# Performance work log

Hardware: AMD Instinct MI355X
Metric: run time of the kernel (lower is better)

The kernel has to match this reference:

```python
import jax, jax.numpy as jnp
import numpy as np

N_NODES = 50000
N_GRAPHS = 64


def _gcn_layer(x, w, b, src, dst, dinv):
    # GCNConv: out = D^{-1/2} (A+I) D^{-1/2} (x W) + b; self-loops already in src/dst
    xw = x @ w                                  # [N, out]
    norm = (dinv[src] * dinv[dst])[:, None]     # [E+N, 1]
    msgs = xw[src] * norm                       # gather + scale
    out = jax.ops.segment_sum(msgs, dst, num_segments=N_NODES)
    return out + b


def setup_inputs() -> dict:
    key = jax.random.key(0)
    ks = jax.random.split(key, 12)
    E = 800000
    F_IN, H = 128, 256
    x = jax.random.normal(ks[0], (N_NODES, F_IN), dtype=jnp.float32)
    edge_attr = jax.random.normal(ks[1], (E, 4), dtype=jnp.float32)
    edge_index = jax.random.randint(ks[2], (2, E), 0, N_NODES, dtype=jnp.int64)
    batch = jnp.sort(jax.random.randint(ks[3], (N_NODES,), 0, N_GRAPHS, dtype=jnp.int64))
    def glorot(k, fi, fo):
        s = jnp.sqrt(6.0 / (fi + fo))
        return jax.random.uniform(k, (fi, fo), minval=-s, maxval=s, dtype=jnp.float32)
    return {
        "x": x, "edge_attr": edge_attr, "edge_index": edge_index, "batch": batch,
        "w1": glorot(ks[4], F_IN, H), "b1": jnp.zeros((H,), jnp.float32),
        "w2": glorot(ks[5], H, H), "b2": jnp.zeros((H,), jnp.float32),
        "w3": glorot(ks[6], H, H), "b3": jnp.zeros((H,), jnp.float32),
        "lin1_w": glorot(ks[7], H, H // 2), "lin1_b": jnp.zeros((H // 2,), jnp.float32),
        "lin2_w": glorot(ks[8], H // 2, 3), "lin2_b": jnp.zeros((3,), jnp.float32),
    }


def reference(x, edge_attr, edge_index, batch, w1, b1, w2, b2, w3, b3,
              lin1_w, lin1_b, lin2_w, lin2_b):
    # add self-loops once; shared by all three conv layers
    loop = jnp.arange(N_NODES, dtype=edge_index.dtype)
    src = jnp.concatenate([edge_index[0], loop])
    dst = jnp.concatenate([edge_index[1], loop])
    deg = jax.ops.segment_sum(jnp.ones_like(dst, dtype=x.dtype), dst, num_segments=N_NODES)
    dinv = jnp.where(deg > 0, jax.lax.rsqrt(deg), 0.0)

    h = jax.nn.relu(_gcn_layer(x, w1, b1, src, dst, dinv))
    h = jax.nn.relu(_gcn_layer(h, w2, b2, src, dst, dinv))
    h = _gcn_layer(h, w3, b3, src, dst, dinv)

    # global mean pool over graphs
    sums = jax.ops.segment_sum(h, batch, num_segments=N_GRAPHS)
    cnts = jax.ops.segment_sum(jnp.ones((h.shape[0],), h.dtype), batch, num_segments=N_GRAPHS)
    pooled = sums / jnp.maximum(cnts, 1.0)[:, None]

    # eval mode: dropout is identity
    out = pooled @ lin1_w + lin1_b
    out = out @ lin2_w + lin2_b
    return out
```

## Files before the change

kernel.cpp:

```cpp
#include <hip/hip_runtime.h>
#include <cstdint>

constexpr int NG = 64;
constexpr int H  = 256;

typedef __bf16 bf16x8 __attribute__((ext_vector_type(8)));
typedef float  f32x4  __attribute__((ext_vector_type(4)));

__device__ __forceinline__ uint32_t pk_bf16(float a, float b) {
    uint32_t ua = __builtin_bit_cast(uint32_t, a);
    uint32_t ub = __builtin_bit_cast(uint32_t, b);
    ua += 0x7fffu + ((ua >> 16) & 1u);
    ub += 0x7fffu + ((ub >> 16) & 1u);
    return (ua >> 16) | (ub & 0xffff0000u);
}
__device__ __forceinline__ ushort bf16r(float x) {
    uint32_t u = __builtin_bit_cast(uint32_t, x);
    u += 0x7fffu + ((u >> 16) & 1u);
    return (ushort)(u >> 16);
}
__device__ __forceinline__ float bf2f(ushort h) {
    return __builtin_bit_cast(float, ((uint32_t)h) << 16);
}
__device__ __forceinline__ void bf2acc(uint32_t u, float& a0, float& a1) {
    a0 += __builtin_bit_cast(float, u << 16);
    a1 += __builtin_bit_cast(float, u & 0xffff0000u);
}

__global__ void hist_kernel(const int* __restrict__ dst, int* __restrict__ cnt, int E) {
    int e = blockIdx.x * blockDim.x + threadIdx.x;
    if (e < E) atomicAdd(&cnt[dst[e]], 1);
}

__global__ __launch_bounds__(256) void scanA(const int* __restrict__ cnt, int* __restrict__ bsum,
                                             float* __restrict__ dinv, int n) {
    __shared__ int sh[256];
    int t = threadIdx.x, i = blockIdx.x * 256 + t;
    int v = (i < n) ? cnt[i] : 0;
    if (i < n) dinv[i] = rsqrtf((float)(v + 1));
    sh[t] = v;
    __syncthreads();
    for (int off = 128; off > 0; off >>= 1) {
        if (t < off) sh[t] += sh[t + off];
        __syncthreads();
    }
    if (t == 0) bsum[blockIdx.x] = sh[0];
}

__global__ __launch_bounds__(256) void scanB(const int* __restrict__ bsum, int* __restrict__ boff,
                                             int* __restrict__ total_out, int nb,
                                             float* __restrict__ sums, int* __restrict__ gcnt) {
    __shared__ int sh[256];
    int t = threadIdx.x;
    for (int i = t; i < NG * H; i += 256) sums[i] = 0.f;
    if (t < NG) gcnt[t] = 0;
    int v = (t < nb) ? bsum[t] : 0;
    sh[t] = v;
    __syncthreads();
    for (int off = 1; off < 256; off <<= 1) {
        int a = (t >= off) ? sh[t - off] : 0;
        __syncthreads();
        sh[t] += a;
        __syncthreads();
    }
    if (t < nb) boff[t] = sh[t] - v;
    if (t == nb - 1) *total_out = sh[t];
}

__global__ __launch_bounds__(256) void scanC(const int* __restrict__ cnt, const int* __restrict__ boff,
                                             int* __restrict__ row_ptr, int* __restrict__ fill, int n) {
    __shared__ int sh[256];
    int t = threadIdx.x, i = blockIdx.x * 256 + t;
    int v = (i < n) ? cnt[i] : 0;
    sh[t] = v;
    __syncthreads();
    for (int off = 1; off < 256; off <<= 1) {
        int a = (t >= off) ? sh[t - off] : 0;
        __syncthreads();
        sh[t] += a;
        __syncthreads();
    }
    if (i < n) {
        int excl = boff[blockIdx.x] + sh[t] - v;
        row_ptr[i] = excl;
        fill[i] = excl;
    }
}

constexpr int WCONV_BLOCKS = (128 * 256 + 256 * 256) / 256;
__global__ void wsp_kernel(const float* __restrict__ w1, ushort* __restrict__ h1, ushort* __restrict__ l1,
                           const float* __restrict__ w2, ushort* __restrict__ h2, ushort* __restrict__ l2,
                           const int* __restrict__ src, const int* __restrict__ dst,
                           int* __restrict__ fill, ushort* __restrict__ ssrc, int E,
                           const float* __restrict__ x, const float* __restrict__ dinv,
                           ushort* __restrict__ y, int N) {
    if (blockIdx.x < WCONV_BLOCKS) {
        int idx = blockIdx.x * 256 + threadIdx.x;
        const float* w; ushort *hi, *lo; int K;
        if (idx < 128 * 256) { w = w1; hi = h1; lo = l1; K = 128; }
        else { idx -= 128 * 256; w = w2; hi = h2; lo = l2; K = 256; }
        int k = idx / 256, n = idx & 255;
        float v = w[idx];
        ushort h = bf16r(v);
        float r = v - bf2f(h);
        hi[n * K + k] = h;
        lo[n * K + k] = bf16r(r);
        return;
    }
    int i = (blockIdx.x - WCONV_BLOCKS) * 256 + threadIdx.x;
    if (i < E) {
        int pos = atomicAdd(&fill[dst[i]], 1);
        ssrc[pos] = (ushort)src[i];
    }
    int np4 = N * 32;
    if (i < np4) {
        int f = i * 4;
        int node = f >> 7;
        int k = f & 127;
        float dv = dinv[node];
        float4 v = *reinterpret_cast<const float4*>(x + f);
        uint2 o;
        o.x = pk_bf16(v.x * dv, v.y * dv);
        o.y = pk_bf16(v.z * dv, v.w * dv);
        *reinterpret_cast<uint2*>(y + ((size_t)(k >> 5) * N + node) * 32 + (k & 31)) = o;
    }
}

template<int NC>
__global__ __launch_bounds__(256) void agg_kernel(const ushort* __restrict__ y,
                                                  const float* __restrict__ dinv,
                                                  const int* __restrict__ row_ptr,
                                                  const ushort* __restrict__ ssrc,
                                                  ushort* __restrict__ zout, int n) {
    int wave = threadIdx.x >> 6;
    int lane = threadIdx.x & 63;
    int grp  = lane >> 3;
    int fd   = lane & 7;
    int chunk = blockIdx.x % NC;
    int node  = (blockIdx.x / NC) * 32 + wave * 8 + grp;
    if (node >= n) return;
    const ushort* yc = y + (size_t)chunk * n * 32;

    float a0, a1, a2, a3;
    {
        uint2 u = *reinterpret_cast<const uint2*>(yc + (size_t)node * 32 + fd * 4);
        a0 = a1 = a2 = a3 = 0.f;
        bf2acc(u.x, a0, a1); bf2acc(u.y, a2, a3);
    }
    int beg = row_ptr[node], end = row_ptr[node + 1];
    int e = beg;
    for (; e + 2 <= end; e += 2) {
        int s0 = ssrc[e], s1 = ssrc[e + 1];
        uint2 u0 = *reinterpret_cast<const uint2*>(yc + (size_t)s0 * 32 + fd * 4);
        uint2 u1 = *reinterpret_cast<const uint2*>(yc + (size_t)s1 * 32 + fd * 4);
        bf2acc(u0.x, a0, a1); bf2acc(u0.y, a2, a3);
        bf2acc(u1.x, a0, a1); bf2acc(u1.y, a2, a3);
    }
    if (e < end) {
        int s = ssrc[e];
        uint2 u = *reinterpret_cast<const uint2*>(yc + (size_t)s * 32 + fd * 4);
        bf2acc(u.x, a0, a1); bf2acc(u.y, a2, a3);
    }
    float dv = dinv[node];
    uint2 o;
    o.x = pk_bf16(dv * a0, dv * a1);
    o.y = pk_bf16(dv * a2, dv * a3);
    *reinterpret_cast<uint2*>(zout + ((size_t)chunk * n + node) * 32 + fd * 4) = o;
}

template<bool RELU>
__global__ __launch_bounds__(256) void mfma_gemm(const ushort* __restrict__ A,
                                                 const ushort* __restrict__ Bhi,
                                                 const ushort* __restrict__ Blo,
                                                 const float* __restrict__ bias,
                                                 const float* __restrict__ dinv,
                                                 ushort* __restrict__ C, int M, int K) {
    constexpr int BM = 128, BN = 64, BK = 64;
    constexpr int LDK = BK + 8;
    __shared__ ushort As[BM][LDK];
    __shared__ ushort Bh[BN][LDK];
    __shared__ ushort Bl[BN][LDK];

    const int tid = threadIdx.x;
    const int w = tid >> 6;
    const int l = tid & 63;
    const int lr = l & 15;
    const int lk = (l >> 4) * 8;
    const int bm = blockIdx.x * BM;
    const int bn = blockIdx.y * BN;

    f32x4 acc[8];
    #pragma unroll
    for (int i = 0; i < 8; ++i) acc[i] = (f32x4){0.f, 0.f, 0.f, 0.f};

    for (int k0 = 0; k0 < K; k0 += BK) {
        #pragma unroll
        for (int p = 0; p < 4; ++p) {
            int g = tid + p * 256;
            int r = g >> 3;
            int c = (g & 7) << 3;
            int grow = bm + r;
            int gk = k0 + c;
            uint4 va = make_uint4(0u, 0u, 0u, 0u);
            if (grow < M)
                va = *reinterpret_cast<const uint4*>(A + ((size_t)(gk >> 5) * M + grow) * 32 + (gk & 31));
            *reinterpret_cast<uint4*>(&As[r][c]) = va;
        }
        #pragma unroll
        for (int p = 0; p < 2; ++p) {
            int g = tid + p * 256;
            int r = g >> 3;
            int c = (g & 7) << 3;
            *reinterpret_cast<uint4*>(&Bh[r][c]) =
                *reinterpret_cast<const uint4*>(Bhi + (size_t)(bn + r) * K + k0 + c);
            *reinterpret_cast<uint4*>(&Bl[r][c]) =
                *reinterpret_cast<const uint4*>(Blo + (size_t)(bn + r) * K + k0 + c);
        }
        __syncthreads();
        #pragma unroll
        for (int kk = 0; kk < BK; kk += 32) {
            bf16x8 bh = *reinterpret_cast<const bf16x8*>(&Bh[w * 16 + lr][kk + lk]);
            bf16x8 bl = *reinterpret_cast<const bf16x8*>(&Bl[w * 16 + lr][kk + lk]);
            #pragma unroll
            for (int r16 = 0; r16 < 8; ++r16) {
                bf16x8 a = *reinterpret_cast<const bf16x8*>(&As[r16 * 16 + lr][kk + lk]);
                acc[r16] = __builtin_amdgcn_mfma_f32_16x16x32_bf16(a, bh, acc[r16], 0, 0, 0);
                acc[r16] = __builtin_amdgcn_mfma_f32_16x16x32_bf16(a, bl, acc[r16], 0, 0, 0);
            }
        }
        __syncthreads();
    }

    int col = bn + w * 16 + lr;
    int cc = col >> 5, co = col & 31;
    float bv = bias[col];
    #pragma unroll
    for (int r16 = 0; r16 < 8; ++r16) {
        #pragma unroll
        for (int j = 0; j < 4; ++j) {
            int row = bm + r16 * 16 + (l >> 4) * 4 + j;
            if (row < M) {
                float v = acc[r16][j] + bv;
                if (RELU) v = fmaxf(v, 0.f);
                v *= dinv[row];
                C[((size_t)cc * M + row) * 32 + co] = bf16r(v);
            }
        }
    }
}

__global__ __launch_bounds__(256) void pool_kernel(const ushort* __restrict__ z,
                                                   const int* __restrict__ batch,
                                                   float* __restrict__ sums,
                                                   int* __restrict__ gcnt, int n) {
    constexpr int NCH = 128;
    int t = threadIdx.x;
    int base = blockIdx.x * NCH;
    if (base >= n) return;
    int endn = min(base + NCH, n);
    size_t poff = (size_t)(t >> 5) * n;
    int co = t & 31;
    int cur = batch[base];
    float local = 0.f;
    int cl = 0;
    for (int i = base; i < endn; ++i) {
        int g = batch[i];
        if (g != cur) {
            atomicAdd(&sums[cur * H + t], local);
            if (t == 0) atomicAdd(&gcnt[cur], cl);
            local = 0.f; cl = 0; cur = g;
        }
        local += bf2f(z[(poff + i) * 32 + co]);
        cl++;
    }
    atomicAdd(&sums[cur * H + t], local);
    if (t == 0) atomicAdd(&gcnt[cur], cl);
}

__global__ __launch_bounds__(256) void head_kernel(const float* __restrict__ sums,
                                                   const int* __restrict__ gcnt,
                                                   const float* __restrict__ w3, const float* __restrict__ b3,
                                                   const float* __restrict__ l1w, const float* __restrict__ l1b,
                                                   const float* __restrict__ l2w, const float* __restrict__ l2b,
                                                   float* __restrict__ out) {
    __shared__ float pooled[H];
    __shared__ float t3[H];
    __shared__ float mid[H / 2];
    int g = blockIdx.x, t = threadIdx.x;
    float c = (float)max(gcnt[g], 1);
    pooled[t] = sums[g * H + t] / c;
    __syncthreads();
    float a = b3[t];
    for (int k = 0; k < H; ++k) a += pooled[k] * w3[k * H + t];
    t3[t] = a;
    __syncthreads();
    if (t < H / 2) {
        float m = l1b[t];
        for (int k = 0; k < H; ++k) m += t3[k] * l1w[k * (H / 2) + t];
        mid[t] = m;
    }
    __syncthreads();
    if (t < 3) {
        float o = l2b[t];
        for (int k = 0; k < H / 2; ++k) o += mid[k] * l2w[k * 3 + t];
        out[g * 3 + t] = o;
    }
}

extern "C" void kernel_launch(void* const* d_in, const int* in_sizes, int n_in,
                              void* d_out, int out_size, void* d_ws, size_t ws_size,
                              hipStream_t stream) {
    const float* x   = (const float*)d_in[0];
    const int*   ei  = (const int*)d_in[2];
    const int*   bat = (const int*)d_in[3];
    const float* w1  = (const float*)d_in[4];
    const float* b1  = (const float*)d_in[5];
    const float* w2  = (const float*)d_in[6];
    const float* b2  = (const float*)d_in[7];
    const float* w3  = (const float*)d_in[8];
    const float* b3  = (const float*)d_in[9];
    const float* l1w = (const float*)d_in[10];
    const float* l1b = (const float*)d_in[11];
    const float* l2w = (const float*)d_in[12];
    const float* l2b = (const float*)d_in[13];
    float* out = (float*)d_out;

    const int N = in_sizes[0] / 128;
    const int E = in_sizes[2] / 2;
    const int NB = (N + 255) / 256;

    char* ws = (char*)d_ws;
    size_t off = 0;
    auto alloc = [&](size_t bytes) {
        void* p = ws + off;
        off = (off + bytes + 255) & ~(size_t)255;
        return p;
    };
    ushort* yb     = (ushort*)alloc((size_t)N * H * 2);
    ushort* z16    = (ushort*)alloc((size_t)N * H * 2);
    int*    cnt    = (int*)alloc((size_t)N * 4);
    float*  dinv   = (float*)alloc((size_t)N * 4);
    int*    row_ptr= (int*)alloc((size_t)(N + 1) * 4);
    int*    fill   = (int*)alloc((size_t)N * 4);
    ushort* ssrc   = (ushort*)alloc((size_t)E * 2);
    int*    bsum   = (int*)alloc(256 * 4);
    int*    boff   = (int*)alloc(256 * 4);
    ushort* wt1h   = (ushort*)alloc((size_t)128 * 256 * 2);
    ushort* wt1l   = (ushort*)alloc((size_t)128 * 256 * 2);
    ushort* wt2h   = (ushort*)alloc((size_t)256 * 256 * 2);
    ushort* wt2l   = (ushort*)alloc((size_t)256 * 256 * 2);
    float*  sums   = (float*)alloc((size_t)NG * H * 4);
    int*    gcnt   = (int*)alloc((size_t)NG * 4);

    hipMemsetAsync(cnt, 0, (size_t)N * 4, stream);

    hist_kernel<<<(E + 255) / 256, 256, 0, stream>>>(ei + E, cnt, E);
    scanA<<<NB, 256, 0, stream>>>(cnt, bsum, dinv, N);
    scanB<<<1, 256, 0, stream>>>(bsum, boff, row_ptr + N, NB, sums, gcnt);
    scanC<<<NB, 256, 0, stream>>>(cnt, boff, row_ptr, fill, N);
    int sp_blocks = (N * 32 + 255) / 256;
    wsp_kernel<<<WCONV_BLOCKS + sp_blocks, 256, 0, stream>>>(
        w1, wt1h, wt1l, w2, wt2h, wt2l,
        ei, ei + E, fill, ssrc, E, x, dinv, yb, N);

    const int AGG_BLOCKS = (N + 31) / 32;
    agg_kernel<4><<<AGG_BLOCKS * 4, 256, 0, stream>>>(yb, dinv, row_ptr, ssrc, z16, N);
    mfma_gemm<true><<<dim3((N + 127) / 128, 4), 256, 0, stream>>>(z16, wt1h, wt1l, b1, dinv, yb, N, 128);

    agg_kernel<8><<<AGG_BLOCKS * 8, 256, 0, stream>>>(yb, dinv, row_ptr, ssrc, z16, N);
    mfma_gemm<true><<<dim3((N + 127) / 128, 4), 256, 0, stream>>>(z16, wt2h, wt2l, b2, dinv, yb, N, 256);

    agg_kernel<8><<<AGG_BLOCKS * 8, 256, 0, stream>>>(yb, dinv, row_ptr, ssrc, z16, N);

    pool_kernel<<<(N + 127) / 128, 256, 0, stream>>>(z16, bat, sums, gcnt, N);
    head_kernel<<<NG, 256, 0, stream>>>(sums, gcnt, w3, b3, l1w, l1b, l2w, l2b, out);
}
```

Measured before the change: 470.5 us.

## Fuse all GCN stages into one persistent cooperative kernel with grid syncs

Result: slower. 1.450 ms (+208.2%).

```diff
diff --git a/kernel.cpp b/kernel.cpp
--- a/kernel.cpp
+++ b/kernel.cpp
@@ -1,5 +1,8 @@
 #include <hip/hip_runtime.h>
+#include <hip/hip_cooperative_groups.h>
 #include <cstdint>
+
+namespace cg = cooperative_groups;
 
 constexpr int NG = 64;
 constexpr int H  = 256;
@@ -27,351 +30,310 @@
     a1 += __builtin_bit_cast(float, u & 0xffff0000u);
 }
 
-__global__ void hist_kernel(const int* __restrict__ dst, int* __restrict__ cnt, int E) {
-    int e = blockIdx.x * blockDim.x + threadIdx.x;
-    if (e < E) atomicAdd(&cnt[dst[e]], 1);
-}
-
-__global__ __launch_bounds__(256) void scanA(const int* __restrict__ cnt, int* __restrict__ bsum,
-                                             float* __restrict__ dinv, int n) {
-    __shared__ int sh[256];
-    int t = threadIdx.x, i = blockIdx.x * 256 + t;
-    int v = (i < n) ? cnt[i] : 0;
-    if (i < n) dinv[i] = rsqrtf((float)(v + 1));
-    sh[t] = v;
-    __syncthreads();
-    for (int off = 128; off > 0; off >>= 1) {
-        if (t < off) sh[t] += sh[t + off];
-        __syncthreads();
-    }
-    if (t == 0) bsum[blockIdx.x] = sh[0];
-}
-
-__global__ __launch_bounds__(256) void scanB(const int* __restrict__ bsum, int* __restrict__ boff,
-                                             int* __restrict__ total_out, int nb,
-                                             float* __restrict__ sums, int* __restrict__ gcnt) {
-    __shared__ int sh[256];
-    int t = threadIdx.x;
-    for (int i = t; i < NG * H; i += 256) sums[i] = 0.f;
-    if (t < NG) gcnt[t] = 0;
-    int v = (t < nb) ? bsum[t] : 0;
-    sh[t] = v;
-    __syncthreads();
-    for (int off = 1; off < 256; off <<= 1) {
-        int a = (t >= off) ? sh[t - off] : 0;
-        __syncthreads();
-        sh[t] += a;
-        __syncthreads();
-    }
-    if (t < nb) boff[t] = sh[t] - v;
-    if (t == nb - 1) *total_out = sh[t];
-}
-
-__global__ __launch_bounds__(256) void scanC(const int* __restrict__ cnt, const int* __restrict__ boff,
-                                             int* __restrict__ row_ptr, int* __restrict__ fill, int n) {
-    __shared__ int sh[256];
-    int t = threadIdx.x, i = blockIdx.x * 256 + t;
-    int v = (i < n) ? cnt[i] : 0;
-    sh[t] = v;
-    __syncthreads();
-    for (int off = 1; off < 256; off <<= 1) {
-        int a = (t >= off) ? sh[t - off] : 0;
-        __syncthreads();
-        sh[t] += a;
-        __syncthreads();
-    }
-    if (i < n) {
-        int excl = boff[blockIdx.x] + sh[t] - v;
-        row_ptr[i] = excl;
-        fill[i] = excl;
-    }
-}
-
-constexpr int WCONV_BLOCKS = (128 * 256 + 256 * 256) / 256;
-__global__ void wsp_kernel(const float* __restrict__ w1, ushort* __restrict__ h1, ushort* __restrict__ l1,
-                           const float* __restrict__ w2, ushort* __restrict__ h2, ushort* __restrict__ l2,
-                           const int* __restrict__ src, const int* __restrict__ dst,
-                           int* __restrict__ fill, ushort* __restrict__ ssrc, int E,
-                           const float* __restrict__ x, const float* __restrict__ dinv,
-                           ushort* __restrict__ y, int N) {
-    if (blockIdx.x < WCONV_BLOCKS) {
-        int idx = blockIdx.x * 256 + threadIdx.x;
+struct Params {
+    const float* x; const int* ei; const int* bat;
+    const float* w1; const float* b1; const float* w2; const float* b2;
+    const float* w3; const float* b3;
+    const float* l1w; const float* l1b; const float* l2w; const float* l2b;
+    float* out;
+    int N, E, NB;
+    int* cnt; float* dinv; int* row_ptr; int* fill;
+    ushort* ssrc; int* bsum; int* boff;
+    ushort* yb; ushort* z16;
+    ushort* wt1h; ushort* wt1l; ushort* wt2h; ushort* wt2l;
+};
+
+union SMem {
+    int scan[256];
+    struct { ushort As[64][72]; ushort Bh[64][72]; ushort Bl[64][72]; } g;
+    struct { float pooled[256]; float t3[256]; float mid[128]; } h;
+};
+
+__device__ __forceinline__ int lower_bound(const int* a, int n, int v) {
+    int lo = 0, hi = n;
+    while (lo < hi) { int m = (lo + hi) >> 1; if (a[m] < v) lo = m + 1; else hi = m; }
+    return lo;
+}
+
+template<int NC>
+__device__ void agg_phase(const Params& p, const ushort* __restrict__ y,
+                          ushort* __restrict__ z) {
+    int wave = threadIdx.x >> 6, lane = threadIdx.x & 63;
+    int grp = lane >> 3, fd = lane & 7;
+    int nvb = ((p.N + 31) / 32) * NC;
+    for (int vb = blockIdx.x; vb < nvb; vb += gridDim.x) {
+        int chunk = vb % NC;
+        int node = (vb / NC) * 32 + wave * 8 + grp;
+        if (node >= p.N) continue;
+        const ushort* yc = y + (size_t)chunk * p.N * 32;
+        float a0 = 0.f, a1 = 0.f, a2 = 0.f, a3 = 0.f;
+        {
+            uint2 u = *reinterpret_cast<const uint2*>(yc + (size_t)node * 32 + fd * 4);
+            bf2acc(u.x, a0, a1); bf2acc(u.y, a2, a3);
+        }
+        int beg = p.row_ptr[node], end = p.row_ptr[node + 1];
+        int e = beg;
+        for (; e + 2 <= end; e += 2) {
+            int s0 = p.ssrc[e], s1 = p.ssrc[e + 1];
+            uint2 u0 = *reinterpret_cast<const uint2*>(yc + (size_t)s0 * 32 + fd * 4);
+            uint2 u1 = *reinterpret_cast<const uint2*>(yc + (size_t)s1 * 32 + fd * 4);
+            bf2acc(u0.x, a0, a1); bf2acc(u0.y, a2, a3);
+            bf2acc(u1.x, a0, a1); bf2acc(u1.y, a2, a3);
+        }
+        if (e < end) {
+            int s = p.ssrc[e];
+            uint2 u = *reinterpret_cast<const uint2*>(yc + (size_t)s * 32 + fd * 4);
+            bf2acc(u.x, a0, a1); bf2acc(u.y, a2, a3);
+        }
+        float dv = p.dinv[node];
+        uint2 o;
+        o.x = pk_bf16(dv * a0, dv * a1);
+        o.y = pk_bf16(dv * a2, dv * a3);
+        *reinterpret_cast<uint2*>(z + ((size_t)chunk * p.N + node) * 32 + fd * 4) = o;
+    }
+}
+
+__device__ void gemm_phase(const Params& p, SMem& sm, const ushort* __restrict__ A,
+                           const ushort* __restrict__ Bhi, const ushort* __restrict__ Blo,
+                           const float* __restrict__ bias, ushort* __restrict__ C, int K) {
+    const int tid = threadIdx.x;
+    const int w = tid >> 6, l = tid & 63, lr = l & 15, lk = (l >> 4) * 8;
+    const int M = p.N;
+    int ntile = ((M + 63) / 64) * 4;
+    for (int vt = blockIdx.x; vt < ntile; vt += gridDim.x) {
+        int bm = (vt >> 2) * 64;
+        int bn = (vt & 3) * 64;
+        f32x4 acc[4];
+        #pragma unroll
+        for (int i = 0; i < 4; ++i) acc[i] = (f32x4){0.f, 0.f, 0.f, 0.f};
+        for (int k0 = 0; k0 < K; k0 += 64) {
+            #pragma unroll
+            for (int pass = 0; pass < 2; ++pass) {
+                int g = tid + pass * 256;
+                int r = g >> 3, c = (g & 7) << 3;
+                int grow = bm + r, gk = k0 + c;
+                uint4 va = make_uint4(0u, 0u, 0u, 0u);
+                if (grow < M)
+                    va = *reinterpret_cast<const uint4*>(A + ((size_t)(gk >> 5) * M + grow) * 32 + (gk & 31));
+                *reinterpret_cast<uint4*>(&sm.g.As[r][c]) = va;
+                *reinterpret_cast<uint4*>(&sm.g.Bh[r][c]) =
+                    *reinterpret_cast<const uint4*>(Bhi + (size_t)(bn + r) * K + k0 + c);
+                *reinterpret_cast<uint4*>(&sm.g.Bl[r][c]) =
+                    *reinterpret_cast<const uint4*>(Blo + (size_t)(bn + r) * K + k0 + c);
+            }
+            __syncthreads();
+            #pragma unroll
+            for (int kk = 0; kk < 64; kk += 32) {
+                bf16x8 bh = *reinterpret_cast<const bf16x8*>(&sm.g.Bh[w * 16 + lr][kk + lk]);
+                bf16x8 bl = *reinterpret_cast<const bf16x8*>(&sm.g.Bl[w * 16 + lr][kk + lk]);
+                #pragma unroll
+                for (int r16 = 0; r16 < 4; ++r16) {
+                    bf16x8 a = *reinterpret_cast<const bf16x8*>(&sm.g.As[r16 * 16 + lr][kk + lk]);
+                    acc[r16] = __builtin_amdgcn_mfma_f32_16x16x32_bf16(a, bh, acc[r16], 0, 0, 0);
+                    acc[r16] = __builtin_amdgcn_mfma_f32_16x16x32_bf16(a, bl, acc[r16], 0, 0, 0);
+                }
+            }
+            __syncthreads();
+        }
+        int col = bn + w * 16 + lr;
+        int cc = col >> 5, co = col & 31;
+        float bv = bias[col];
+        #pragma unroll
+        for (int r16 = 0; r16 < 4; ++r16) {
+            #pragma unroll
+            for (int j = 0; j < 4; ++j) {
+                int row = bm + r16 * 16 + (l >> 4) * 4 + j;
+                if (row < M) {
+                    float v = acc[r16][j] + bv;
+                    v = fmaxf(v, 0.f);
+                    v *= p.dinv[row];
+                    C[((size_t)cc * M + row) * 32 + co] = bf16r(v);
+                }
+            }
+        }
+    }
+}
+
+constexpr int WCONV_TOT = (128 + 256) * 256;
+
+__global__ __launch_bounds__(256, 4) void mega(Params p) {
+    cg::grid_group grid = cg::this_grid();
+    __shared__ SMem sm;
+    const int tid = threadIdx.x;
+    const int gstride = gridDim.x * 256;
+    const int gthread = blockIdx.x * 256 + tid;
+
+    for (int i = gthread; i < p.N; i += gstride) p.cnt[i] = 0;
+    grid.sync();
+
+    for (int e = gthread; e < p.E; e += gstride) atomicAdd(&p.cnt[p.ei[p.E + e]], 1);
+    for (int idx0 = gthread; idx0 < WCONV_TOT; idx0 += gstride) {
+        int idx = idx0;
         const float* w; ushort *hi, *lo; int K;
-        if (idx < 128 * 256) { w = w1; hi = h1; lo = l1; K = 128; }
-        else { idx -= 128 * 256; w = w2; hi = h2; lo = l2; K = 256; }
+        if (idx < 128 * 256) { w = p.w1; hi = p.wt1h; lo = p.wt1l; K = 128; }
+        else { idx -= 128 * 256; w = p.w2; hi = p.wt2h; lo = p.wt2l; K = 256; }
         int k = idx / 256, n = idx & 255;
         float v = w[idx];
         ushort h = bf16r(v);
-        float r = v - bf2f(h);
         hi[n * K + k] = h;
-        lo[n * K + k] = bf16r(r);
-        return;
-    }
-    int i = (blockIdx.x - WCONV_BLOCKS) * 256 + threadIdx.x;
-    if (i < E) {
-        int pos = atomicAdd(&fill[dst[i]], 1);
-        ssrc[pos] = (ushort)src[i];
-    }
-    int np4 = N * 32;
-    if (i < np4) {
+        lo[n * K + k] = bf16r(v - bf2f(h));
+    }
+    grid.sync();
+
+    for (int vb = blockIdx.x; vb < p.NB; vb += gridDim.x) {
+        int i = vb * 256 + tid;
+        int v = (i < p.N) ? p.cnt[i] : 0;
+        if (i < p.N) p.dinv[i] = rsqrtf((float)(v + 1));
+        sm.scan[tid] = v;
+        __syncthreads();
+        for (int off = 128; off > 0; off >>= 1) {
+            if (tid < off) sm.scan[tid] += sm.scan[tid + off];
+            __syncthreads();
+        }
+        if (tid == 0) p.bsum[vb] = sm.scan[0];
+        __syncthreads();
+    }
+    grid.sync();
+
+    if (blockIdx.x == 0) {
+        int v = (tid < p.NB) ? p.bsum[tid] : 0;
+        sm.scan[tid] = v;
+        __syncthreads();
+        for (int off = 1; off < 256; off <<= 1) {
+            int a = (tid >= off) ? sm.scan[tid - off] : 0;
+            __syncthreads();
+            sm.scan[tid] += a;
+            __syncthreads();
+        }
+        if (tid < p.NB) p.boff[tid] = sm.scan[tid] - v;
+        if (tid == p.NB - 1) p.row_ptr[p.N] = sm.scan[tid];
+    }
+    grid.sync();
+
+    for (int vb = blockIdx.x; vb < p.NB; vb += gridDim.x) {
+        int i = vb * 256 + tid;
+        int v = (i < p.N) ? p.cnt[i] : 0;
+        sm.scan[tid] = v;
+        __syncthreads();
+        for (int off = 1; off < 256; off <<= 1) {
+            int a = (tid >= off) ? sm.scan[tid - off] : 0;
+            __syncthreads();
+            sm.scan[tid] += a;
+            __syncthreads();
+        }
+        if (i < p.N) {
+            int excl = p.boff[vb] + sm.scan[tid] - v;
+            p.row_ptr[i] = excl;
+            p.fill[i] = excl;
+        }
+        __syncthreads();
+    }
+    grid.sync();
+
+    for (int i = gthread; i < p.E; i += gstride) {
+        int pos = atomicAdd(&p.fill[p.ei[p.E + i]], 1);
+        p.ssrc[pos] = (ushort)p.ei[i];
+    }
+    for (int i = gthread; i < p.N * 32; i += gstride) {
         int f = i * 4;
         int node = f >> 7;
         int k = f & 127;
-        float dv = dinv[node];
-        float4 v = *reinterpret_cast<const float4*>(x + f);
+        float dv = p.dinv[node];
+        float4 v = *reinterpret_cast<const float4*>(p.x + f);
         uint2 o;
         o.x = pk_bf16(v.x * dv, v.y * dv);
         o.y = pk_bf16(v.z * dv, v.w * dv);
-        *reinterpret_cast<uint2*>(y + ((size_t)(k >> 5) * N + node) * 32 + (k & 31)) = o;
-    }
-}
-
-template<int NC>
-__global__ __launch_bounds__(256) void agg_kernel(const ushort* __restrict__ y,
-                                                  const float* __restrict__ dinv,
-                                                  const int* __restrict__ row_ptr,
-                                                  const ushort* __restrict__ ssrc,
-                                                  ushort* __restrict__ zout, int n) {
-    int wave = threadIdx.x >> 6;
-    int lane = threadIdx.x & 63;
-    int grp  = lane >> 3;
-    int fd   = lane & 7;
-    int chunk = blockIdx.x % NC;
-    int node  = (blockIdx.x / NC) * 32 + wave * 8 + grp;
-    if (node >= n) return;
-    const ushort* yc = y + (size_t)chunk * n * 32;
-
-    float a0, a1, a2, a3;
-    {
-        uint2 u = *reinterpret_cast<const uint2*>(yc + (size_t)node * 32 + fd * 4);
-        a0 = a1 = a2 = a3 = 0.f;
-        bf2acc(u.x, a0, a1); bf2acc(u.y, a2, a3);
-    }
-    int beg = row_ptr[node], end = row_ptr[node + 1];
-    int e = beg;
-    for (; e + 2 <= end; e += 2) {
-        int s0 = ssrc[e], s1 = ssrc[e + 1];
-        uint2 u0 = *reinterpret_cast<const uint2*>(yc + (size_t)s0 * 32 + fd * 4);
-        uint2 u1 = *reinterpret_cast<const uint2*>(yc + (size_t)s1 * 32 + fd * 4);
-        bf2acc(u0.x, a0, a1); bf2acc(u0.y, a2, a3);
-        bf2acc(u1.x, a0, a1); bf2acc(u1.y, a2, a3);
-    }
-    if (e < end) {
-        int s = ssrc[e];
-        uint2 u = *reinterpret_cast<const uint2*>(yc + (size_t)s * 32 + fd * 4);
-        bf2acc(u.x, a0, a1); bf2acc(u.y, a2, a3);
-    }
-    float dv = dinv[node];
-    uint2 o;
-    o.x = pk_bf16(dv * a0, dv * a1);
-    o.y = pk_bf16(dv * a2, dv * a3);
-    *reinterpret_cast<uint2*>(zout + ((size_t)chunk * n + node) * 32 + fd * 4) = o;
-}
-
-template<bool RELU>
-__global__ __launch_bounds__(256) void mfma_gemm(const ushort* __restrict__ A,
-                                                 const ushort* __restrict__ Bhi,
-                                                 const ushort* __restrict__ Blo,
-                                                 const float* __restrict__ bias,
-                                                 const float* __restrict__ dinv,
-                                                 ushort* __restrict__ C, int M, int K) {
-    constexpr int BM = 128, BN = 64, BK = 64;
-    constexpr int LDK = BK + 8;
-    __shared__ ushort As[BM][LDK];
-    __shared__ ushort Bh[BN][LDK];
-    __shared__ ushort Bl[BN][LDK];
-
-    const int tid = threadIdx.x;
-    const int w = tid >> 6;
-    const int l = tid & 63;
-    const int lr = l & 15;
-    const int lk = (l >> 4) * 8;
-    const int bm = blockIdx.x * BM;
-    const int bn = blockIdx.y * BN;
-
-    f32x4 acc[8];
-    #pragma unroll
-    for (int i = 0; i < 8; ++i) acc[i] = (f32x4){0.f, 0.f, 0.f, 0.f};
-
-    for (int k0 = 0; k0 < K; k0 += BK) {
-        #pragma unroll
-        for (int p = 0; p < 4; ++p) {
-            int g = tid + p * 256;
-            int r = g >> 3;
-            int c = (g & 7) << 3;
-            int grow = bm + r;
-            int gk = k0 + c;
-            uint4 va = make_uint4(0u, 0u, 0u, 0u);
-            if (grow < M)
-                va = *reinterpret_cast<const uint4*>(A + ((size_t)(gk >> 5) * M + grow) * 32 + (gk & 31));
-            *reinterpret_cast<uint4*>(&As[r][c]) = va;
-        }
-        #pragma unroll
-        for (int p = 0; p < 2; ++p) {
-            int g = tid + p * 256;
-            int r = g >> 3;
-            int c = (g & 7) << 3;
-            *reinterpret_cast<uint4*>(&Bh[r][c]) =
-                *reinterpret_cast<const uint4*>(Bhi + (size_t)(bn + r) * K + k0 + c);
-            *reinterpret_cast<uint4*>(&Bl[r][c]) =
-                *reinterpret_cast<const uint4*>(Blo + (size_t)(bn + r) * K + k0 + c);
-        }
-        __syncthreads();
-        #pragma unroll
-        for (int kk = 0; kk < BK; kk += 32) {
-            bf16x8 bh = *reinterpret_cast<const bf16x8*>(&Bh[w * 16 + lr][kk + lk]);
-            bf16x8 bl = *reinterpret_cast<const bf16x8*>(&Bl[w * 16 + lr][kk + lk]);
-            #pragma unroll
-            for (int r16 = 0; r16 < 8; ++r16) {
-                bf16x8 a = *reinterpret_cast<const bf16x8*>(&As[r16 * 16 + lr][kk + lk]);
-                acc[r16] = __builtin_amdgcn_mfma_f32_16x16x32_bf16(a, bh, acc[r16], 0, 0, 0);
-                acc[r16] = __builtin_amdgcn_mfma_f32_16x16x32_bf16(a, bl, acc[r16], 0, 0, 0);
-            }
-        }
-        __syncthreads();
-    }
-
-    int col = bn + w * 16 + lr;
-    int cc = col >> 5, co = col & 31;
-    float bv = bias[col];
-    #pragma unroll
-    for (int r16 = 0; r16 < 8; ++r16) {
-        #pragma unroll
-        for (int j = 0; j < 4; ++j) {
-            int row = bm + r16 * 16 + (l >> 4) * 4 + j;
-            if (row < M) {
-                float v = acc[r16][j] + bv;
-                if (RELU) v = fmaxf(v, 0.f);
-                v *= dinv[row];
-                C[((size_t)cc * M + row) * 32 + co] = bf16r(v);
-            }
-        }
-    }
-}
-
-__global__ __launch_bounds__(256) void pool_kernel(const ushort* __restrict__ z,
-                                                   const int* __restrict__ batch,
-                                                   float* __restrict__ sums,
-                                                   int* __restrict__ gcnt, int n) {
-    constexpr int NCH = 128;
-    int t = threadIdx.x;
-    int base = blockIdx.x * NCH;
-    if (base >= n) return;
-    int endn = min(base + NCH, n);
-    size_t poff = (size_t)(t >> 5) * n;
-    int co = t & 31;
-    int cur = batch[base];
-    float local = 0.f;
-    int cl = 0;
-    for (int i = base; i < endn; ++i) {
-        int g = batch[i];
-        if (g != cur) {
-            atomicAdd(&sums[cur * H + t], local);
-            if (t == 0) atomicAdd(&gcnt[cur], cl);
-            local = 0.f; cl = 0; cur = g;
-        }
-        local += bf2f(z[(poff + i) * 32 + co]);
-        cl++;
-    }
-    atomicAdd(&sums[cur * H + t], local);
-    if (t == 0) atomicAdd(&gcnt[cur], cl);
-}
-
-__global__ __launch_bounds__(256) void head_kernel(const float* __restrict__ sums,
-                                                   const int* __restrict__ gcnt,
-                                                   const float* __restrict__ w3, const float* __restrict__ b3,
-                                                   const float* __restrict__ l1w, const float* __restrict__ l1b,
-                                                   const float* __restrict__ l2w, const float* __restrict__ l2b,
-                                                   float* __restrict__ out) {
-    __shared__ float pooled[H];
-    __shared__ float t3[H];
-    __shared__ float mid[H / 2];
-    int g = blockIdx.x, t = threadIdx.x;
-    float c = (float)max(gcnt[g], 1);
-    pooled[t] = sums[g * H + t] / c;
-    __syncthreads();
-    float a = b3[t];
-    for (int k = 0; k < H; ++k) a += pooled[k] * w3[k * H + t];
-    t3[t] = a;
-    __syncthreads();
-    if (t < H / 2) {
-        float m = l1b[t];
-        for (int k = 0; k < H; ++k) m += t3[k] * l1w[k * (H / 2) + t];
-        mid[t] = m;
-    }
-    __syncthreads();
-    if (t < 3) {
-        float o = l2b[t];
-        for (int k = 0; k < H / 2; ++k) o += mid[k] * l2w[k * 3 + t];
-        out[g * 3 + t] = o;
+        *reinterpret_cast<uint2*>(p.yb + ((size_t)(k >> 5) * p.N + node) * 32 + (k & 31)) = o;
+    }
+    grid.sync();
+
+    agg_phase<4>(p, p.yb, p.z16);
+    grid.sync();
+    gemm_phase(p, sm, p.z16, p.wt1h, p.wt1l, p.b1, p.yb, 128);
+    grid.sync();
+    agg_phase<8>(p, p.yb, p.z16);
+    grid.sync();
+    gemm_phase(p, sm, p.z16, p.wt2h, p.wt2l, p.b2, p.yb, 256);
+    grid.sync();
+    agg_phase<8>(p, p.yb, p.z16);
+    grid.sync();
+
+    if (blockIdx.x < NG) {
+        int g = blockIdx.x;
+        int lo = lower_bound(p.bat, p.N, g);
+        int hi = lower_bound(p.bat, p.N, g + 1);
+        size_t poff = (size_t)(tid >> 5) * p.N;
+        int co = tid & 31;
+        float s = 0.f;
+        for (int i = lo; i < hi; ++i) s += bf2f(p.z16[(poff + i) * 32 + co]);
+        sm.h.pooled[tid] = s / (float)max(hi - lo, 1);
+        __syncthreads();
+        float a = p.b3[tid];
+        for (int k = 0; k < H; ++k) a += sm.h.pooled[k] * p.w3[k * H + tid];
+        sm.h.t3[tid] = a;
+        __syncthreads();
+        if (tid < H / 2) {
+            float m = p.l1b[tid];
+            for (int k = 0; k < H; ++k) m += sm.h.t3[k] * p.l1w[k * (H / 2) + tid];
+            sm.h.mid[tid] = m;
+        }
+        __syncthreads();
+        if (tid < 3) {
+            float o = p.l2b[tid];
+            for (int k = 0; k < H / 2; ++k) o += sm.h.mid[k] * p.l2w[k * 3 + tid];
+            p.out[g * 3 + tid] = o;
+        }
     }
 }
 
 extern "C" void kernel_launch(void* const* d_in, const int* in_sizes, int n_in,
                               void* d_out, int out_size, void* d_ws, size_t ws_size,
                               hipStream_t stream) {
-    const float* x   = (const float*)d_in[0];
-    const int*   ei  = (const int*)d_in[2];
-    const int*   bat = (const int*)d_in[3];
-    const float* w1  = (const float*)d_in[4];
-    const float* b1  = (const float*)d_in[5];
-    const float* w2  = (const float*)d_in[6];
-    const float* b2  = (const float*)d_in[7];
-    const float* w3  = (const float*)d_in[8];
-    const float* b3  = (const float*)d_in[9];
-    const float* l1w = (const float*)d_in[10];
-    const float* l1b = (const float*)d_in[11];
-    const float* l2w = (const float*)d_in[12];
-    const float* l2b = (const float*)d_in[13];
-    float* out = (float*)d_out;
-
-    const int N = in_sizes[0] / 128;
-    const int E = in_sizes[2] / 2;
-    const int NB = (N + 255) / 256;
+    Params P;
+    P.x   = (const float*)d_in[0];
+    P.ei  = (const int*)d_in[2];
+    P.bat = (const int*)d_in[3];
+    P.w1  = (const float*)d_in[4];  P.b1 = (const float*)d_in[5];
+    P.w2  = (const float*)d_in[6];  P.b2 = (const float*)d_in[7];
+    P.w3  = (const float*)d_in[8];  P.b3 = (const float*)d_in[9];
+    P.l1w = (const float*)d_in[10]; P.l1b = (const float*)d_in[11];
+    P.l2w = (const float*)d_in[12]; P.l2b = (const float*)d_in[13];
+    P.out = (float*)d_out;
+    P.N = in_sizes[0] / 128;
+    P.E = in_sizes[2] / 2;
+    P.NB = (P.N + 255) / 256;
 
     char* ws = (char*)d_ws;
     size_t off = 0;
     auto alloc = [&](size_t bytes) {
-        void* p = ws + off;
+        void* ptr = ws + off;
         off = (off + bytes + 255) & ~(size_t)255;
-        return p;
+        return ptr;
     };
-    ushort* yb     = (ushort*)alloc((size_t)N * H * 2);
-    ushort* z16    = (ushort*)alloc((size_t)N * H * 2);
-    int*    cnt    = (int*)alloc((size_t)N * 4);
-    float*  dinv   = (float*)alloc((size_t)N * 4);
-    int*    row_ptr= (int*)alloc((size_t)(N + 1) * 4);
-    int*    fill   = (int*)alloc((size_t)N * 4);
-    ushort* ssrc   = (ushort*)alloc((size_t)E * 2);
-    int*    bsum   = (int*)alloc(256 * 4);
-    int*    boff   = (int*)alloc(256 * 4);
-    ushort* wt1h   = (ushort*)alloc((size_t)128 * 256 * 2);
-    ushort* wt1l   = (ushort*)alloc((size_t)128 * 256 * 2);
-    ushort* wt2h   = (ushort*)alloc((size_t)256 * 256 * 2);
-    ushort* wt2l   = (ushort*)alloc((size_t)256 * 256 * 2);
-    float*  sums   = (float*)alloc((size_t)NG * H * 4);
-    int*    gcnt   = (int*)alloc((size_t)NG * 4);
-
-    hipMemsetAsync(cnt, 0, (size_t)N * 4, stream);
-
-    hist_kernel<<<(E + 255) / 256, 256, 0, stream>>>(ei + E, cnt, E);
-    scanA<<<NB, 256, 0, stream>>>(cnt, bsum, dinv, N);
-    scanB<<<1, 256, 0, stream>>>(bsum, boff, row_ptr + N, NB, sums, gcnt);
-    scanC<<<NB, 256, 0, stream>>>(cnt, boff, row_ptr, fill, N);
-    int sp_blocks = (N * 32 + 255) / 256;
-    wsp_kernel<<<WCONV_BLOCKS + sp_blocks, 256, 0, stream>>>(
-        w1, wt1h, wt1l, w2, wt2h, wt2l,
-        ei, ei + E, fill, ssrc, E, x, dinv, yb, N);
-
-    const int AGG_BLOCKS = (N + 31) / 32;
-    agg_kernel<4><<<AGG_BLOCKS * 4, 256, 0, stream>>>(yb, dinv, row_ptr, ssrc, z16, N);
-    mfma_gemm<true><<<dim3((N + 127) / 128, 4), 256, 0, stream>>>(z16, wt1h, wt1l, b1, dinv, yb, N, 128);
-
-    agg_kernel<8><<<AGG_BLOCKS * 8, 256, 0, stream>>>(yb, dinv, row_ptr, ssrc, z16, N);
-    mfma_gemm<true><<<dim3((N + 127) / 128, 4), 256, 0, stream>>>(z16, wt2h, wt2l, b2, dinv, yb, N, 256);
-
-    agg_kernel<8><<<AGG_BLOCKS * 8, 256, 0, stream>>>(yb, dinv, row_ptr, ssrc, z16, N);
-
-    pool_kernel<<<(N + 127) / 128, 256, 0, stream>>>(z16, bat, sums, gcnt, N);
-    head_kernel<<<NG, 256, 0, stream>>>(sums, gcnt, w3, b3, l1w, l1b, l2w, l2b, out);
-}
+    P.yb      = (ushort*)alloc((size_t)P.N * H * 2);
+    P.z16     = (ushort*)alloc((size_t)P.N * H * 2);
+    P.cnt     = (int*)alloc((size_t)P.N * 4);
+    P.dinv    = (float*)alloc((size_t)P.N * 4);
+    P.row_ptr = (int*)alloc((size_t)(P.N + 1) * 4);
+    P.fill    = (int*)alloc((size_t)P.N * 4);
+    P.ssrc    = (ushort*)alloc((size_t)P.E * 2);
+    P.bsum    = (int*)alloc(256 * 4);
+    P.boff    = (int*)alloc(256 * 4);
+    P.wt1h    = (ushort*)alloc((size_t)128 * 256 * 2);
+    P.wt1l    = (ushort*)alloc((size_t)128 * 256 * 2);
+    P.wt2h    = (ushort*)alloc((size_t)256 * 256 * 2);
+    P.wt2l    = (ushort*)alloc((size_t)256 * 256 * 2);
+
+    int blocksPerCU = 0;
+    hipOccupancyMaxActiveBlocksPerMultiprocessor(&blocksPerCU, mega, 256, 0);
+    int numCU = 0, dev = 0;
+    hipGetDevice(&dev);
+    hipDeviceGetAttribute(&numCU, hipDeviceAttributeMultiprocessorCount, dev);
+    int grid = blocksPerCU * numCU;
+    if (grid <= 0) grid = 1024;
+    grid &= ~7;
+    if (grid < 64) grid = 64;
+
+    void* args[] = { &P };
+    hipLaunchCooperativeKernel(mega, dim3(grid), dim3(256), args, 0, stream);
+}
```
